# Optimization experiments

Hardware: AMD Instinct MI355X
Metric: run time of the kernel (lower is better)

The kernel has to match this reference:

```python
import jax, jax.numpy as jnp
import numpy as np

# open-unmix Separator constants (n_fft=4096, hop=1024 defaults of umxhq)
N_FFT = 4096
N_HOP = 1024
WIENER_WIN = 300   # wiener_win_len
NITER = 1          # EM iterations
EPS = 1e-10
SCALE_FACTOR = 10.0
B, T_FRAMES, N_BINS, N_CH, N_SRC = 2, 600, 2049, 2, 4
AUDIO_LEN = (T_FRAMES - 1) * N_HOP  # center=True STFT framing -> 613376


def _invert2x2(C):
    # closed-form inverse of (..., 2, 2) complex matrices (as in openunmix _invert)
    det = C[..., 0, 0] * C[..., 1, 1] - C[..., 0, 1] * C[..., 1, 0]
    row0 = jnp.stack([C[..., 1, 1], -C[..., 0, 1]], axis=-1)
    row1 = jnp.stack([-C[..., 1, 0], C[..., 0, 0]], axis=-1)
    return jnp.stack([row0, row1], axis=-2) / det[..., None, None]


def _em_step(y, x, eps):
    # y: (T,F,C,S) complex source estimates, x: (T,F,C) complex mixture
    C = x.shape[-1]
    # power spectral densities, averaged over channels: (T,F,S)
    v = jnp.mean(jnp.abs(y) ** 2, axis=2)
    # spatial covariance per source, pooled over frames: (F,S,C,C)
    R_num = jnp.einsum('tfas,tfbs->fsab', y, jnp.conj(y))
    weight = eps + jnp.sum(v, axis=0)  # (F,S)
    R = R_num / weight[..., None, None].astype(R_num.dtype)
    reg = jnp.sqrt(jnp.asarray(eps, jnp.float32)) * jnp.eye(C, dtype=x.dtype)
    # mixture covariance model: (T,F,C,C)
    Cxx = reg + jnp.einsum('tfs,fsab->tfab', v, R)
    inv_x = jnp.einsum('tfab,tfb->tfa', _invert2x2(Cxx), x)  # Cxx^{-1} x
    # y_j = v_j R_j Cxx^{-1} x  (multichannel Wiener gain applied to mixture)
    y_new = jnp.einsum('tfs,fsab,tfb->tfas', v, R, inv_x)
    return y_new


def _wiener(spec, mix):
    # spec: (T,F,C,S) float magnitudes, mix: (T,F,C) complex
    # initial estimates: target magnitude with mixture phase (softmask=False path)
    y = spec.astype(jnp.complex64) * jnp.exp(1j * jnp.angle(mix))[..., None]
    max_abs = jnp.maximum(jnp.asarray(1.0, jnp.float32),
                          jnp.sqrt(jnp.max(jnp.abs(mix) ** 2)) / SCALE_FACTOR)
    mix_s = mix / max_abs
    y = y / max_abs
    for _ in range(NITER):
        y = _em_step(y, mix_s, EPS)
    return y * max_abs


def _istft(Y, n_fft, hop, length):
    # Y: (..., F, T) complex onesided spectra -> (..., length) real audio
    batch = Y.shape[:-2]
    T = Y.shape[-1]
    frames = jnp.fft.irfft(Y, n=n_fft, axis=-2)  # (..., n_fft, T)
    n = jnp.arange(n_fft)
    win = 0.5 - 0.5 * jnp.cos(2.0 * jnp.pi * n / n_fft)  # periodic hann
    frames = frames * win[:, None].astype(frames.dtype)
    frames = jnp.moveaxis(frames, -2, -1).reshape(-1, T, n_fft)  # (Bf, T, n_fft)
    out_len = n_fft + hop * (T - 1)
    idx = (jnp.arange(T) * hop)[:, None] + n[None, :]  # (T, n_fft)
    out = jnp.zeros((frames.shape[0], out_len), frames.dtype).at[:, idx].add(frames)
    wsum = jnp.zeros((out_len,), jnp.float32).at[idx].add(
        jnp.broadcast_to(win ** 2, (T, n_fft)))
    out = out / jnp.where(wsum > 1e-11, wsum, 1.0)
    start = n_fft // 2  # undo center padding
    out = out[:, start:start + length]
    return out.reshape(*batch, length)


def setup_inputs() -> dict:
    key = jax.random.key(0)
    k1, k2 = jax.random.split(key)
    spectrograms = jax.random.uniform(k1, (B, T_FRAMES, N_BINS, N_CH, N_SRC),
                                      dtype=jnp.float32)
    mix_stft = jax.random.normal(k2, (B, T_FRAMES, N_BINS, N_CH, 2),
                                 dtype=jnp.float32)
    return {"spectrograms": spectrograms, "mix_stft": mix_stft}


def reference(spectrograms, mix_stft):
    mix = mix_stft[..., 0] + 1j * mix_stft[..., 1]  # (B,T,F,C) complex64
    W = T_FRAMES // WIENER_WIN
    spec_w = spectrograms.reshape(B * W, WIENER_WIN, N_BINS, N_CH, N_SRC)
    mix_w = mix.reshape(B * W, WIENER_WIN, N_BINS, N_CH)
    y = jax.vmap(_wiener)(spec_w, mix_w)  # (B*W, T_w, F, C, S)
    y = y.reshape(B, T_FRAMES, N_BINS, N_CH, N_SRC)
    # -> (B, S, C, F, T) as in Separator's permute before istft
    Y = jnp.transpose(y, (0, 4, 3, 2, 1))
    estimates = _istft(Y, N_FFT, N_HOP, AUDIO_LEN)  # (B, S, C, L)
    return estimates
```

## Files before the change

kernel.cpp:

```cpp
#include <hip/hip_runtime.h>
#include <hip/hip_fp16.h>

#define NB 2049
#define TF 600
#define WINF 300
#define NFFT 4096
#define HOP 1024
#define ALEN 613376
#define EPSV 1e-10f
#define SQEPS 1e-5f
#define RCH 10
#define RCHT 30
#define ROWH2 2050
#define W4096 0.0015339807878856412f

#define PADI(i) ((i) + ((i) >> 4))

__device__ __forceinline__ float2 cmul(float2 a, float2 b) {
  return make_float2(a.x*b.x - a.y*b.y, a.x*b.y + a.y*b.x);
}
__device__ __forceinline__ float2 cadd(float2 a, float2 b) {
  return make_float2(a.x + b.x, a.y + b.y);
}
__device__ __forceinline__ float2 csub(float2 a, float2 b) {
  return make_float2(a.x - b.x, a.y - b.y);
}

__device__ __forceinline__ float2 h2f2(unsigned w) {
  union { unsigned u; __half2 h; } c; c.u = w;
  return __half22float2(c.h);
}

__global__ __launch_bounds__(256) void k_init(unsigned int* c2max) {
  if (blockIdx.x == 0 && threadIdx.x < 4) c2max[threadIdx.x] = 0u;
}

__global__ __launch_bounds__(256) void k_maxred(const float* __restrict__ mix,
                                                unsigned int* __restrict__ c2max) {
  int winid = blockIdx.x >> 6;
  int blk = blockIdx.x & 63;
  const float4* p = (const float4*)(mix + (size_t)winid * (WINF * NB * 2 * 2));
  const int n4 = WINF * NB * 2 * 2 / 4;
  float m = 0.f;
  for (int i = blk * 256 + threadIdx.x; i < n4; i += 64 * 256) {
    float4 v = p[i];
    m = fmaxf(m, fmaxf(v.x*v.x + v.y*v.y, v.z*v.z + v.w*v.w));
  }
  for (int off = 32; off; off >>= 1) m = fmaxf(m, __shfl_xor(m, off));
  __shared__ float sm[4];
  if ((threadIdx.x & 63) == 0) sm[threadIdx.x >> 6] = m;
  __syncthreads();
  if (threadIdx.x == 0) {
    m = fmaxf(fmaxf(sm[0], sm[1]), fmaxf(sm[2], sm[3]));
    atomicMax(c2max + winid, __float_as_uint(m));
  }
}

__global__ __launch_bounds__(256) void k_rmat_part(const float* __restrict__ spec,
                                                   const float* __restrict__ mix,
                                                   float* __restrict__ part,
                                                   unsigned int* __restrict__ c2max) {
  int ftile = blockIdx.x % 9;
  int chunk = (blockIdx.x / 9) % RCH;
  int winid = blockIdx.x / (9 * RCH);
  int f = ftile * 256 + threadIdx.x;
  const bool act = (f < NB);
  int b = winid >> 1, w = winid & 1;
  float acc[16];
#pragma unroll
  for (int i = 0; i < 16; i++) acc[i] = 0.f;
  float mx2 = 0.f;
  if (act) {
    for (int tt = 0; tt < RCHT; tt++) {
      int t = w * WINF + chunk * RCHT + tt;
      size_t base = (size_t)(b * TF + t) * NB + f;
      const float4* sp = (const float4*)(spec + base * 8);
      float4 s0 = sp[0], s1 = sp[1];
      float4 mx = *(const float4*)(mix + base * 4);
      float n0 = mx.x*mx.x + mx.y*mx.y;
      float n1 = mx.z*mx.z + mx.w*mx.w;
      mx2 = fmaxf(mx2, fmaxf(n0, n1));
      float qr, qi;
      if (n0 > 0.f && n1 > 0.f) {
        float inv = rsqrtf(n0 * n1);
        qr = (mx.x*mx.z + mx.y*mx.w) * inv;
        qi = (mx.y*mx.z - mx.x*mx.w) * inv;
      } else if (n0 > 0.f) { float inv = rsqrtf(n0); qr = mx.x*inv; qi = mx.y*inv; }
      else if (n1 > 0.f)   { float inv = rsqrtf(n1); qr = mx.z*inv; qi = -mx.w*inv; }
      else { qr = 1.f; qi = 0.f; }
      float A0[4] = {s0.x, s0.y, s0.z, s0.w};
      float A1[4] = {s1.x, s1.y, s1.z, s1.w};
#pragma unroll
      for (int s = 0; s < 4; s++) {
        acc[s*4+0] += A0[s]*A0[s];
        acc[s*4+1] += A1[s]*A1[s];
        float aa = A0[s]*A1[s];
        acc[s*4+2] += aa * qr;
        acc[s*4+3] += aa * qi;
      }
    }
    float* pp = part + (((size_t)winid * RCH + chunk) * NB + f) * 16;
#pragma unroll
    for (int s = 0; s < 4; s++)
      *(float4*)(pp + s*4) = make_float4(acc[s*4+0], acc[s*4+1], acc[s*4+2], acc[s*4+3]);
  }
  for (int off = 32; off; off >>= 1) mx2 = fmaxf(mx2, __shfl_xor(mx2, off));
  __shared__ float sm[4];
  if ((threadIdx.x & 63) == 0) sm[threadIdx.x >> 6] = mx2;
  __syncthreads();
  if (threadIdx.x == 0) {
    mx2 = fmaxf(fmaxf(sm[0], sm[1]), fmaxf(sm[2], sm[3]));
    atomicMax(c2max + winid, __float_as_uint(mx2));
  }
}

__global__ __launch_bounds__(256) void k_rmat_red(const float* __restrict__ part,
                                                  const unsigned int* __restrict__ c2max,
                                                  float* __restrict__ Rbuf) {
  int idx = blockIdx.x * 256 + threadIdx.x;
  if (idx >= 4 * NB * 4) return;
  int s = idx & 3;
  int f = (idx >> 2) % NB;
  int winid = idx / (NB * 4);
  float4 a = make_float4(0.f, 0.f, 0.f, 0.f);
#pragma unroll
  for (int ch = 0; ch < RCH; ch++) {
    float4 p = *(const float4*)(part + (((size_t)winid * RCH + ch) * NB + f) * 16 + s * 4);
    a.x += p.x; a.y += p.y; a.z += p.z; a.w += p.w;
  }
  float c = fmaxf(1.f, sqrtf(__uint_as_float(c2max[winid])) * 0.1f);
  float W = c * c * EPSV + 0.5f * (a.x + a.y);
  float invW = 1.f / W;
  *(float4*)(Rbuf + ((size_t)winid * NB + f) * 16 + s * 4) =
      make_float4(a.x*invW, a.y*invW, a.z*invW, a.w*invW);
}

__global__ __launch_bounds__(256) void k_rmat(const float* __restrict__ spec,
                                              const float* __restrict__ mix,
                                              const unsigned int* __restrict__ c2max,
                                              float* __restrict__ Rbuf) {
  int f = blockIdx.x;
  int winid = threadIdx.x >> 6;
  int lane = threadIdx.x & 63;
  int b = winid >> 1, w = winid & 1;
  float acc[16];
#pragma unroll
  for (int i = 0; i < 16; i++) acc[i] = 0.f;
  for (int tl = lane; tl < WINF; tl += 64) {
    int t = w * WINF + tl;
    size_t base = (size_t)(b * TF + t) * NB + f;
    const float4* sp = (const float4*)(spec + base * 8);
    float4 s0 = sp[0], s1 = sp[1];
    float4 mx = *(const float4*)(mix + base * 4);
    float n0 = mx.x*mx.x + mx.y*mx.y;
    float n1 = mx.z*mx.z + mx.w*mx.w;
    float qr, qi;
    if (n0 > 0.f && n1 > 0.f) {
      float inv = rsqrtf(n0 * n1);
      qr = (mx.x*mx.z + mx.y*mx.w) * inv;
      qi = (mx.y*mx.z - mx.x*mx.w) * inv;
    } else if (n0 > 0.f) { float inv = rsqrtf(n0); qr = mx.x*inv; qi = mx.y*inv; }
    else if (n1 > 0.f)   { float inv = rsqrtf(n1); qr = mx.z*inv; qi = -mx.w*inv; }
    else { qr = 1.f; qi = 0.f; }
    float A0[4] = {s0.x, s0.y, s0.z, s0.w};
    float A1[4] = {s1.x, s1.y, s1.z, s1.w};
#pragma unroll
    for (int s = 0; s < 4; s++) {
      acc[s*4+0] += A0[s]*A0[s];
      acc[s*4+1] += A1[s]*A1[s];
      float aa = A0[s]*A1[s];
      acc[s*4+2] += aa * qr;
      acc[s*4+3] += aa * qi;
    }
  }
#pragma unroll
  for (int i = 0; i < 16; i++) {
#pragma unroll
    for (int off = 32; off; off >>= 1) acc[i] += __shfl_xor(acc[i], off);
  }
  if (lane == 0) {
    float c = fmaxf(1.f, sqrtf(__uint_as_float(c2max[winid])) * 0.1f);
    float c2 = c * c;
#pragma unroll
    for (int s = 0; s < 4; s++) {
      float W = c2 * EPSV + 0.5f * (acc[s*4+0] + acc[s*4+1]);
      float invW = 1.f / W;
      *(float4*)(Rbuf + ((size_t)winid * NB + f) * 16 + s * 4) =
          make_float4(acc[s*4+0]*invW, acc[s*4+1]*invW, acc[s*4+2]*invW, acc[s*4+3]*invW);
    }
  }
}

__global__ __launch_bounds__(256) void k_apply(const float* __restrict__ spec,
                                               const float* __restrict__ mix,
                                               const unsigned int* __restrict__ c2max,
                                               const float* __restrict__ Rbuf,
                                               __half2* __restrict__ Y) {
  size_t idx = (size_t)blockIdx.x * 256 + threadIdx.x;
  if (idx >= (size_t)2 * TF * NB) return;
  int f = (int)(idx % NB);
  int r = (int)(idx / NB);
  int t = r % TF, b = r / TF;
  int winid = b * 2 + (t >= WINF ? 1 : 0);
  float c = fmaxf(1.f, sqrtf(__uint_as_float(c2max[winid])) * 0.1f);
  float invc = 1.f / c, inv2c2 = 0.5f * invc * invc;
  size_t base = (size_t)(b * TF + t) * NB + f;
  const float4* sp = (const float4*)(spec + base * 8);
  float4 s0v = sp[0], s1v = sp[1];
  float4 mx = *(const float4*)(mix + base * 4);
  const float4* Rp = (const float4*)(Rbuf + ((size_t)winid * NB + f) * 16);
  float A0[4] = {s0v.x, s0v.y, s0v.z, s0v.w};
  float A1[4] = {s1v.x, s1v.y, s1v.z, s1v.w};
  float v[4]; float4 R[4];
  float C00 = SQEPS, C11 = SQEPS, C01r = 0.f, C01i = 0.f;
#pragma unroll
  for (int sq = 0; sq < 4; sq++) {
    R[sq] = Rp[sq];
    v[sq] = (A0[sq]*A0[sq] + A1[sq]*A1[sq]) * inv2c2;
    C00 += v[sq]*R[sq].x; C11 += v[sq]*R[sq].y;
    C01r += v[sq]*R[sq].z; C01i += v[sq]*R[sq].w;
  }
  float det = C00*C11 - (C01r*C01r + C01i*C01i);
  float invdet = 1.f / det;
  float x0r = mx.x*invc, x0i = mx.y*invc, x1r = mx.z*invc, x1i = mx.w*invc;
  float ix0r = (C11*x0r - (C01r*x1r - C01i*x1i)) * invdet;
  float ix0i = (C11*x0i - (C01r*x1i + C01i*x1r)) * invdet;
  float ix1r = (C00*x1r - (C01r*x0r + C01i*x0i)) * invdet;
  float ix1i = (C00*x1i - (C01r*x0i - C01i*x0r)) * invdet;
#pragma unroll
  for (int sq = 0; sq < 4; sq++) {
    float vc = v[sq] * c;
    float y0r = vc*(R[sq].x*ix0r + R[sq].z*ix1r - R[sq].w*ix1i);
    float y0i = vc*(R[sq].x*ix0i + R[sq].z*ix1i + R[sq].w*ix1r);
    float y1r = vc*(R[sq].z*ix0r + R[sq].w*ix0i + R[sq].y*ix1r);
    float y1i = vc*(R[sq].z*ix0i - R[sq].w*ix0r + R[sq].y*ix1i);
    size_t r0 = ((size_t)(((b * 4 + sq) * 2) * TF) + t) * ROWH2 + f;
    Y[r0] = __floats2half2_rn(y0r, y0i);
    Y[r0 + (size_t)TF * ROWH2] = __floats2half2_rn(y1r, y1i);
  }
}

__device__ __forceinline__ void dft8(const float2* x, float2* X) {
  const float S2 = 0.70710678118654752f;
  float2 t0 = cadd(x[0], x[4]), t1 = csub(x[0], x[4]);
  float2 t2 = cadd(x[2], x[6]), t3 = csub(x[2], x[6]);
  float2 E0 = cadd(t0, t2), E2 = csub(t0, t2);
  float2 E1 = make_float2(t1.x - t3.y, t1.y + t3.x);
  float2 E3 = make_float2(t1.x + t3.y, t1.y - t3.x);
  float2 u0 = cadd(x[1], x[5]), u1 = csub(x[1], x[5]);
  float2 u2 = cadd(x[3], x[7]), u3 = csub(x[3], x[7]);
  float2 O0 = cadd(u0, u2), O2 = csub(u0, u2);
  float2 O1 = make_float2(u1.x - u3.y, u1.y + u3.x);
  float2 O3 = make_float2(u1.x + u3.y, u1.y - u3.x);
  float2 R1 = make_float2(S2*(O1.x - O1.y), S2*(O1.x + O1.y));
  float2 R2 = make_float2(-O2.y, O2.x);
  float2 R3 = make_float2(-S2*(O3.x + O3.y), S2*(O3.x - O3.y));
  X[0] = cadd(E0, O0); X[4] = csub(E0, O0);
  X[1] = cadd(E1, R1); X[5] = csub(E1, R1);
  X[2] = cadd(E2, R2); X[6] = csub(E2, R2);
  X[3] = cadd(E3, R3); X[7] = csub(E3, R3);
}

__device__ __forceinline__ void r8_reg(const float2* x, float2* dst, int tid) {
  float2 X[8];
  dft8(x, X);
  const int d = tid << 3;
#pragma unroll
  for (int n = 0; n < 8; n++) dst[PADI(d + n)] = X[n];
}

template<int NS>
__device__ __forceinline__ void r8stage(const float2* __restrict__ src,
                                        float2* __restrict__ dst, int tid) {
  const int q = tid;
  const int jm = q & (NS - 1);
  float2 x[8];
#pragma unroll
  for (int m = 0; m < 8; m++) x[m] = src[PADI(q + (m << 8))];
  {
    float sn, cs;
    __sincosf((float)jm * (0.78539816339744831f / (float)NS), &sn, &cs);
    const float2 w = make_float2(cs, sn);
    float2 wp = w;
    x[1] = cmul(x[1], wp);
#pragma unroll
    for (int m = 2; m < 8; m++) { wp = cmul(wp, w); x[m] = cmul(x[m], wp); }
  }
  float2 X[8];
  dft8(x, X);
  const int d = ((q - jm) << 3) + jm;
#pragma unroll
  for (int n = 0; n < 8; n++) dst[PADI(d + n * NS)] = X[n];
}

__device__ __forceinline__ void r4_final(const float2* __restrict__ src,
                                         __half2* __restrict__ frow, int tid) {
  const float S2 = 0.70710678118654752f;
  float we[8], wo[8];
  float bsn, bcs;
  __sincosf((float)tid * 0.0030679615757712823f , &bsn, &bcs);
  {
    float cs = bcs, sn = bsn;
    const float CD = 0.9999988234517019f, SD = 0.0015339801862847657f;
#pragma unroll
    for (int m = 0; m < 8; m++) {
      we[m] = (0.5f - 0.5f*cs) * (1.f/2048.f);
      float c1 = cs*CD - sn*SD;
      wo[m] = (0.5f - 0.5f*c1) * (1.f/2048.f);
      float ncs = (cs - sn) * S2;
      float nsn = (sn + cs) * S2;
      cs = ncs; sn = nsn;
    }
  }
  float2 w1 = make_float2(bcs, bsn);
#pragma unroll
  for (int qq = 0; qq < 2; qq++) {
    const int q = tid + (qq << 8);
    float2 v0 = src[PADI(q)];
    float2 v1 = src[PADI(q + 512)];
    float2 v2 = src[PADI(q + 1024)];
    float2 v3 = src[PADI(q + 1536)];
    float2 w2 = cmul(w1, w1);
    float2 w3 = cmul(w2, w1);
    v1 = cmul(v1, w1);
    v2 = cmul(v2, w2);
    v3 = cmul(v3, w3);
    float2 t0 = cadd(v0, v2), t1 = csub(v0, v2);
    float2 t2 = cadd(v1, v3), t3 = csub(v1, v3);
    float2 X0 = cadd(t0, t2);
    float2 X1 = make_float2(t1.x - t3.y, t1.y + t3.x);
    float2 X2 = csub(t0, t2);
    float2 X3 = make_float2(t1.x + t3.y, t1.y - t3.x);
    frow[q]        = __floats2half2_rn(X0.x*we[qq],     X0.y*wo[qq]);
    frow[q + 512]  = __floats2half2_rn(X1.x*we[qq + 2], X1.y*wo[qq + 2]);
    frow[q + 1024] = __floats2half2_rn(X2.x*we[qq + 4], X2.y*wo[qq + 4]);
    frow[q + 1536] = __floats2half2_rn(X3.x*we[qq + 6], X3.y*wo[qq + 6]);
    if (qq == 0)
      w1 = make_float2((w1.x - w1.y) * S2, (w1.y + w1.x) * S2);
  }
}

__global__ __launch_bounds__(256) void k_frames(__half2* __restrict__ YF) {
  __shared__ float2 bufA[2176];
  __shared__ float2 bufB[2176];
  const int tid = threadIdx.x;
  const int t = blockIdx.x % TF;
  const int sid = blockIdx.x / TF;
  const size_t row = ((size_t)sid * TF + t) * ROWH2;

  const unsigned* Yu = (const unsigned*)(YF + row);
  unsigned* stg = (unsigned*)bufB;
  for (int i = tid; i < NB; i += 256) stg[i] = Yu[i];
  __syncthreads();

  float2 x[8];
  {
    float sn, cs;
    __sincosf((float)tid * 0.0015339807878856412f , &sn, &cs);
    const float R8c = 0.92387953251128676f, R8s = 0.38268343236508977f;
#pragma unroll
    for (int m = 0; m < 8; m++) {
      const int k = tid + (m << 8);
      float2 Xa = h2f2(stg[k]);
      float2 Xb = h2f2(stg[2048 - k]);
      if (k == 0) { Xa.y = 0.f; Xb.y = 0.f; }
      float Sx = Xa.x + Xb.x, Sy = Xa.y - Xb.y;
      float Dx = Xa.x - Xb.x, Dy = Xa.y + Xb.y;
      x[m] = make_float2(0.5f*(Sx - sn*Dx - cs*Dy), 0.5f*(Sy + cs*Dx - sn*Dy));
      float ncs = cs*R8c - sn*R8s, nsn = sn*R8c + cs*R8s;
      cs = ncs; sn = nsn;
    }
  }
  r8_reg(x, bufA, tid);
  __syncthreads();
  r8stage<8>(bufA, bufB, tid);
  __syncthreads();
  r8stage<64>(bufB, bufA, tid);
  __syncthreads();
  r4_final(bufA, YF + row, tid);
}

__global__ __launch_bounds__(256) void k_gather(const __half2* __restrict__ frames,
                                                float* __restrict__ out) {
  const int sid = blockIdx.x / 1198;
  const int o2 = (blockIdx.x % 1198) * 256 + threadIdx.x;
  const int n = 2048 + 2 * o2;
  const int tbase = n >> 10;
  float sx = 0.f, sy = 0.f;
#pragma unroll
  for (int dt = 0; dt < 4; dt++) {
    int t = tbase - 3 + dt;
    if ((unsigned)t < (unsigned)TF) {
      int j2 = (n - (t << 10)) >> 1;
      float2 v = __half22float2(frames[((size_t)sid * TF + t) * ROWH2 + j2]);
      sx += v.x; sy += v.y;
    }
  }
  float ise, iso;
  if (tbase >= 3 && tbase <= 599) {
    ise = iso = 2.f / 3.f;
  } else {
    float we = 0.f, wo = 0.f;
#pragma unroll
    for (int dt = 0; dt < 4; dt++) {
      int t = tbase - 3 + dt;
      if ((unsigned)t < (unsigned)TF) {
        int j = n - (t << 10);
        float a = 0.5f - 0.5f * __cosf((float)j * W4096);
        float bq = 0.5f - 0.5f * __cosf((float)(j + 1) * W4096);
        we += a * a; wo += bq * bq;
      }
    }
    ise = 1.f / ((we > 1e-11f) ? we : 1.f);
    iso = 1.f / ((wo > 1e-11f) ? wo : 1.f);
  }
  *(float2*)(out + (size_t)sid * ALEN + 2 * o2) = make_float2(sx * ise, sy * iso);
}

__device__ __forceinline__ float2 em_point_one(const float* __restrict__ spec,
    const float* __restrict__ mix, const float* __restrict__ Rbuf,
    const unsigned int* __restrict__ c2max, int b, int t, int f, int ssel, int ch) {
  int winid = b * 2 + (t >= WINF ? 1 : 0);
  float c = fmaxf(1.f, sqrtf(__uint_as_float(c2max[winid])) * 0.1f);
  float invc = 1.f / c, inv2c2 = 0.5f * invc * invc;
  size_t base = (size_t)(b * TF + t) * NB + f;
  const float4* sp = (const float4*)(spec + base * 8);
  float4 s0 = sp[0], s1 = sp[1];
  float4 mx = *(const float4*)(mix + base * 4);
  const float4* Rp = (const float4*)(Rbuf + ((size_t)winid * NB + f) * 16);
  float A0v[4] = {s0.x, s0.y, s0.z, s0.w};
  float A1v[4] = {s1.x, s1.y, s1.z, s1.w};
  float C00 = SQEPS, C11 = SQEPS, C01r = 0.f, C01i = 0.f;
  float vsel = 0.f; float4 Rsel = make_float4(0.f, 0.f, 0.f, 0.f);
#pragma unroll
  for (int sq = 0; sq < 4; sq++) {
    float4 R = Rp[sq];
    float v = (A0v[sq]*A0v[sq] + A1v[sq]*A1v[sq]) * inv2c2;
    C00 += v*R.x; C11 += v*R.y; C01r += v*R.z; C01i += v*R.w;
    if (sq == ssel) { vsel = v; Rsel = R; }
  }
  float det = C00*C11 - (C01r*C01r + C01i*C01i);
  float invdet = 1.f / det;
  float x0r = mx.x*invc, x0i = mx.y*invc, x1r = mx.z*invc, x1i = mx.w*invc;
  float ix0r = (C11*x0r - (C01r*x1r - C01i*x1i)) * invdet;
  float ix0i = (C11*x0i - (C01r*x1i + C01i*x1r)) * invdet;
  float ix1r = (C00*x1r - (C01r*x0r + C01i*x0i)) * invdet;
  float ix1i = (C00*x1i - (C01r*x0i - C01i*x0r)) * invdet;
  float vc = vsel * c;
  if (ch == 0)
    return make_float2(vc*(Rsel.x*ix0r + Rsel.z*ix1r - Rsel.w*ix1i),
                       vc*(Rsel.x*ix0i + Rsel.z*ix1i + Rsel.w*ix1r));
  return make_float2(vc*(Rsel.z*ix0r + Rsel.w*ix0i + Rsel.y*ix1r),
                     vc*(Rsel.z*ix0i - Rsel.w*ix0r + Rsel.y*ix1i));
}

template<int NS>
__device__ __forceinline__ void r4stage(const float2* __restrict__ src,
                                        float2* __restrict__ dst, int tid) {
#pragma unroll
  for (int qq = 0; qq < 2; qq++) {
    int q = tid + qq * 256;
    int jm = q & (NS - 1);
    float2 v0 = src[PADI(q)];
    float2 v1 = src[PADI(q + 512)];
    float2 v2 = src[PADI(q + 1024)];
    float2 v3 = src[PADI(q + 1536)];
    if constexpr (NS > 1) {
      float sn, cs;
      __sincosf((float)jm * (1.5707963267948966f / (float)NS), &sn, &cs);
      float2 w1 = make_float2(cs, sn);
      float2 w2 = cmul(w1, w1);
      float2 w3 = cmul(w2, w1);
      v1 = cmul(v1, w1);
      v2 = cmul(v2, w2);
      v3 = cmul(v3, w3);
    }
    float2 a0 = cadd(v0, v2), a1 = csub(v0, v2);
    float2 a2 = cadd(v1, v3), a3 = csub(v1, v3);
    int d = ((q - jm) << 2) + jm;
    dst[PADI(d)]        = cadd(a0, a2);
    dst[PADI(d + NS)]   = make_float2(a1.x - a3.y, a1.y + a3.x);
    dst[PADI(d + 2*NS)] = csub(a0, a2);
    dst[PADI(d + 3*NS)] = make_float2(a1.x + a3.y, a1.y - a3.x);
  }
}

__device__ __forceinline__ void r2stage(const float2* __restrict__ src,
                                        float2* __restrict__ dst, int tid) {
#pragma unroll
  for (int qq = 0; qq < 4; qq++) {
    int q = tid + qq * 256;
    float sn, cs;
    __sincosf((float)q * 0.003067961575771282f, &sn, &cs);
    float2 v0 = src[PADI(q)];
    float2 v1 = cmul(src[PADI(q + 1024)], make_float2(cs, sn));
    dst[PADI(q)]        = cadd(v0, v1);
    dst[PADI(q + 1024)] = csub(v0, v1);
  }
}

__global__ __launch_bounds__(256) void k_istft_fused(const float* __restrict__ spec,
        const float* __restrict__ mix, const unsigned int* __restrict__ c2max,
        const float* __restrict__ Rbuf, float* __restrict__ out) {
  __shared__ float2 bufA[2176];
  __shared__ float2 bufB[2176];
  const int tid = threadIdx.x;
  const int u = blockIdx.x % 150;
  const int sid = blockIdx.x / 150;
  const int b = sid >> 3;
  const int s = (sid >> 1) & 3;
  const int ch = sid & 1;
  float acc[16], wsm[16];
#pragma unroll
  for (int k = 0; k < 16; k++) { acc[k] = 0.f; wsm[k] = 0.f; }
  const int t0 = max(0, 4 * u - 1);
  const int t1 = min(TF - 1, 4 * u + 5);
  const int M0 = 2048 + u * 4096;
  for (int t = t0; t <= t1; ++t) {
    for (int k = tid; k < 2048; k += 256) {
      float2 Xa = em_point_one(spec, mix, Rbuf, c2max, b, t, k, s, ch);
      float2 Xb = em_point_one(spec, mix, Rbuf, c2max, b, t, 2048 - k, s, ch);
      if (k == 0) { Xa.y = 0.f; Xb.y = 0.f; }
      float Sx = Xa.x + Xb.x, Sy = Xa.y - Xb.y;
      float Dx = Xa.x - Xb.x, Dy = Xa.y + Xb.y;
      float sn, cs;
      __sincosf((float)k * 0.0015339807878856412f, &sn, &cs);
      bufA[PADI(k)] = make_float2(0.5f * (Sx - sn*Dx - cs*Dy),
                                  0.5f * (Sy + cs*Dx - sn*Dy));
    }
    __syncthreads();
    r4stage<1>(bufA, bufB, tid);   __syncthreads();
    r4stage<4>(bufB, bufA, tid);   __syncthreads();
    r4stage<16>(bufA, bufB, tid);  __syncthreads();
    r4stage<64>(bufB, bufA, tid);  __syncthreads();
    r4stage<256>(bufA, bufB, tid); __syncthreads();
    r2stage(bufB, bufA, tid);      __syncthreads();
    const int delta = M0 - t * HOP;
#pragma unroll
    for (int k2 = 0; k2 < 16; k2++) {
      int n = tid + 256 * k2 + delta;
      if (n >= 0 && n < NFFT) {
        float2 z = bufA[PADI(n >> 1)];
        float xn = (n & 1) ? z.y : z.x;
        float wn = 0.5f - 0.5f * __cosf((float)n * W4096);
        acc[k2] += xn * wn * (1.f / 2048.f);
        wsm[k2] += wn * wn;
      }
    }
    __syncthreads();
  }
#pragma unroll
  for (int k2 = 0; k2 < 16; k2++) {
    size_t o = (size_t)u * 4096 + tid + 256 * k2;
    if (o < (size_t)ALEN) {
      float wsv = wsm[k2];
      out[(size_t)sid * ALEN + o] = acc[k2] / (wsv > 1e-11f ? wsv : 1.f);
    }
  }
}

extern "C" void kernel_launch(void* const* d_in, const int* in_sizes, int n_in,
                              void* d_out, int out_size, void* d_ws, size_t ws_size,
                              hipStream_t stream) {
  const float* spec = (const float*)d_in[0];
  const float* mix  = (const float*)d_in[1];
  float* out = (float*)d_out;
  unsigned char* ws = (unsigned char*)d_ws;
  unsigned int* c2max = (unsigned int*)ws;
  float* Rbuf = (float*)(ws + 256);
  __half2* Y = (__half2*)(ws + 524800);
  float* part = (float*)(ws + 524800);
  const size_t needY = 524800 + (size_t)16 * TF * ROWH2 * 4;

  k_init<<<1, 256, 0, stream>>>(c2max);
  if (ws_size >= needY) {
    k_rmat_part<<<4 * RCH * 9, 256, 0, stream>>>(spec, mix, part, c2max);
    k_rmat_red<<<(4 * NB * 4 + 255) / 256, 256, 0, stream>>>(part, c2max, Rbuf);
    int total = 2 * TF * NB;
    k_apply<<<(total + 255) / 256, 256, 0, stream>>>(spec, mix, c2max, Rbuf, Y);
    k_frames<<<16 * TF, 256, 0, stream>>>(Y);
    k_gather<<<16 * 1198, 256, 0, stream>>>(Y, out);
  } else {
    k_maxred<<<256, 256, 0, stream>>>(mix, c2max);
    k_rmat<<<NB, 256, 0, stream>>>(spec, mix, c2max, Rbuf);
    k_istft_fused<<<16 * 150, 256, 0, stream>>>(spec, mix, c2max, Rbuf, out);
  }
}
```

Before: 142.1 us.

## Use single in-place FFT buffer, direct global loads, wider gather, retune rmat chunks

k_frames now uses one shared buffer with in-place radix-8 stages (an extra barrier between reading and writing) and reads the half2 spectrum straight from global memory instead of staging it in LDS. This halves LDS use so more blocks fit per CU, with a launch-bounds occupancy hint. k_gather has each thread produce four outputs with a float4 store, halving the grid. The rmat partial-reduction chunking changes from 10x30 to 20x15.

```diff
diff --git a/kernel.cpp b/kernel.cpp
--- a/kernel.cpp
+++ b/kernel.cpp
@@ -9,8 +9,8 @@
 #define ALEN 613376
 #define EPSV 1e-10f
 #define SQEPS 1e-5f
-#define RCH 10
-#define RCHT 30
+#define RCH 20
+#define RCHT 15
 #define ROWH2 2050
 #define W4096 0.0015339807878856412f
 
@@ -270,13 +270,12 @@
 }
 
 template<int NS>
-__device__ __forceinline__ void r8stage(const float2* __restrict__ src,
-                                        float2* __restrict__ dst, int tid) {
+__device__ __forceinline__ void r8stage_ip(float2* __restrict__ buf, int tid) {
   const int q = tid;
   const int jm = q & (NS - 1);
   float2 x[8];
 #pragma unroll
-  for (int m = 0; m < 8; m++) x[m] = src[PADI(q + (m << 8))];
+  for (int m = 0; m < 8; m++) x[m] = buf[PADI(q + (m << 8))];
   {
     float sn, cs;
     __sincosf((float)jm * (0.78539816339744831f / (float)NS), &sn, &cs);
@@ -288,9 +287,10 @@
   }
   float2 X[8];
   dft8(x, X);
+  __syncthreads();
   const int d = ((q - jm) << 3) + jm;
 #pragma unroll
-  for (int n = 0; n < 8; n++) dst[PADI(d + n * NS)] = X[n];
+  for (int n = 0; n < 8; n++) buf[PADI(d + n * NS)] = X[n];
 }
 
 __device__ __forceinline__ void r4_final(const float2* __restrict__ src,
@@ -340,18 +340,13 @@
   }
 }
 
-__global__ __launch_bounds__(256) void k_frames(__half2* __restrict__ YF) {
-  __shared__ float2 bufA[2176];
-  __shared__ float2 bufB[2176];
+__global__ __launch_bounds__(256, 6) void k_frames(__half2* __restrict__ YF) {
+  __shared__ float2 buf[2176];
   const int tid = threadIdx.x;
   const int t = blockIdx.x % TF;
   const int sid = blockIdx.x / TF;
   const size_t row = ((size_t)sid * TF + t) * ROWH2;
-
   const unsigned* Yu = (const unsigned*)(YF + row);
-  unsigned* stg = (unsigned*)bufB;
-  for (int i = tid; i < NB; i += 256) stg[i] = Yu[i];
-  __syncthreads();
 
   float2 x[8];
   {
@@ -361,8 +356,8 @@
 #pragma unroll
     for (int m = 0; m < 8; m++) {
       const int k = tid + (m << 8);
-      float2 Xa = h2f2(stg[k]);
-      float2 Xb = h2f2(stg[2048 - k]);
+      float2 Xa = h2f2(Yu[k]);
+      float2 Xb = h2f2(Yu[2048 - k]);
       if (k == 0) { Xa.y = 0.f; Xb.y = 0.f; }
       float Sx = Xa.x + Xb.x, Sy = Xa.y - Xb.y;
       float Dx = Xa.x - Xb.x, Dy = Xa.y + Xb.y;
@@ -371,50 +366,57 @@
       cs = ncs; sn = nsn;
     }
   }
-  r8_reg(x, bufA, tid);
+  r8_reg(x, buf, tid);
   __syncthreads();
-  r8stage<8>(bufA, bufB, tid);
+  r8stage_ip<8>(buf, tid);
   __syncthreads();
-  r8stage<64>(bufB, bufA, tid);
+  r8stage_ip<64>(buf, tid);
   __syncthreads();
-  r4_final(bufA, YF + row, tid);
+  r4_final(buf, YF + row, tid);
 }
 
 __global__ __launch_bounds__(256) void k_gather(const __half2* __restrict__ frames,
                                                 float* __restrict__ out) {
-  const int sid = blockIdx.x / 1198;
-  const int o2 = (blockIdx.x % 1198) * 256 + threadIdx.x;
-  const int n = 2048 + 2 * o2;
+  const int sid = blockIdx.x / 599;
+  const int o4 = (blockIdx.x % 599) * 256 + threadIdx.x;
+  const int n = 2048 + 4 * o4;
   const int tbase = n >> 10;
-  float sx = 0.f, sy = 0.f;
+  float s0 = 0.f, s1 = 0.f, s2 = 0.f, s3 = 0.f;
 #pragma unroll
   for (int dt = 0; dt < 4; dt++) {
     int t = tbase - 3 + dt;
     if ((unsigned)t < (unsigned)TF) {
       int j2 = (n - (t << 10)) >> 1;
-      float2 v = __half22float2(frames[((size_t)sid * TF + t) * ROWH2 + j2]);
-      sx += v.x; sy += v.y;
-    }
-  }
-  float ise, iso;
+      const __half2* fr = frames + ((size_t)sid * TF + t) * ROWH2 + j2;
+      float2 va = __half22float2(fr[0]);
+      float2 vb = __half22float2(fr[1]);
+      s0 += va.x; s1 += va.y; s2 += vb.x; s3 += vb.y;
+    }
+  }
+  float i0, i1, i2, i3;
   if (tbase >= 3 && tbase <= 599) {
-    ise = iso = 2.f / 3.f;
+    i0 = i1 = i2 = i3 = 2.f / 3.f;
   } else {
-    float we = 0.f, wo = 0.f;
+    float w0 = 0.f, w1 = 0.f, w2 = 0.f, w3 = 0.f;
 #pragma unroll
     for (int dt = 0; dt < 4; dt++) {
       int t = tbase - 3 + dt;
       if ((unsigned)t < (unsigned)TF) {
         int j = n - (t << 10);
-        float a = 0.5f - 0.5f * __cosf((float)j * W4096);
-        float bq = 0.5f - 0.5f * __cosf((float)(j + 1) * W4096);
-        we += a * a; wo += bq * bq;
+        float a0 = 0.5f - 0.5f * __cosf((float)j * W4096);
+        float a1 = 0.5f - 0.5f * __cosf((float)(j + 1) * W4096);
+        float a2 = 0.5f - 0.5f * __cosf((float)(j + 2) * W4096);
+        float a3 = 0.5f - 0.5f * __cosf((float)(j + 3) * W4096);
+        w0 += a0*a0; w1 += a1*a1; w2 += a2*a2; w3 += a3*a3;
       }
     }
-    ise = 1.f / ((we > 1e-11f) ? we : 1.f);
-    iso = 1.f / ((wo > 1e-11f) ? wo : 1.f);
-  }
-  *(float2*)(out + (size_t)sid * ALEN + 2 * o2) = make_float2(sx * ise, sy * iso);
+    i0 = 1.f / ((w0 > 1e-11f) ? w0 : 1.f);
+    i1 = 1.f / ((w1 > 1e-11f) ? w1 : 1.f);
+    i2 = 1.f / ((w2 > 1e-11f) ? w2 : 1.f);
+    i3 = 1.f / ((w3 > 1e-11f) ? w3 : 1.f);
+  }
+  *(float4*)(out + (size_t)sid * ALEN + 4 * o4) =
+      make_float4(s0 * i0, s1 * i1, s2 * i2, s3 * i3);
 }
 
 __device__ __forceinline__ float2 em_point_one(const float* __restrict__ spec,
@@ -579,7 +581,7 @@
     int total = 2 * TF * NB;
     k_apply<<<(total + 255) / 256, 256, 0, stream>>>(spec, mix, c2max, Rbuf, Y);
     k_frames<<<16 * TF, 256, 0, stream>>>(Y);
-    k_gather<<<16 * 1198, 256, 0, stream>>>(Y, out);
+    k_gather<<<16 * 599, 256, 0, stream>>>(Y, out);
   } else {
     k_maxred<<<256, 256, 0, stream>>>(mix, c2max);
     k_rmat<<<NB, 256, 0, stream>>>(spec, mix, c2max, Rbuf);
```

Result: faster. 137.8 us (-3.0%).
